# Kernel tuning notes

Hardware: AMD Instinct MI355X
Metric: run time of the kernel (lower is better)

Reference implementation:

```python
import jax, jax.numpy as jnp
import numpy as np

B, P, G, E = 2, 16, 128, 96
C110, C011, C001 = 4, 2, 1
N, CO = 128, 2

def _pw(x, W, b):
    """1x1 conv of any spatial rank == pointwise channel mixing."""
    y = jnp.einsum('oc,bc...->bo...', W, x)
    return y + b.reshape((1, -1) + (1,) * (y.ndim - 2))

def _hidden(s110, s011, s001, Ws, bs):
    # s110:[B,C,P,G,1]  s011:[B,C,1,G,E]  s001:[B,C,1,1,E]
    # sub-stream order: [110 full, 110 pool-P, 110 pool-G, 011 full, 011 pool-G, 011 pool-E, 001]
    t110 = s110[..., 0]         # [B,C,P,G]
    t011 = s011[:, :, 0]        # [B,C,G,E]
    t001 = s001[:, :, 0, 0]     # [B,C,E]
    s = (_pw(t110, Ws[0], bs[0])[..., None]
         + _pw(t110.max(axis=2), Ws[1], bs[1])[:, :, None, :, None]
         + _pw(t110.max(axis=3), Ws[2], bs[2])[:, :, :, None, None]
         + _pw(t011, Ws[3], bs[3])[:, :, None, :, :]
         + _pw(t011.max(axis=2), Ws[4], bs[4])[:, :, None, None, :]
         + _pw(t011.max(axis=3), Ws[5], bs[5])[:, :, None, :, None]
         + _pw(t001, Ws[6], bs[6])[:, :, None, None, :])
    s = jax.nn.leaky_relu(s)    # [B,N,P,G,E]
    return (jnp.max(s, axis=4, keepdims=True),
            jnp.max(s, axis=2, keepdims=True),
            jnp.max(s, axis=(2, 3), keepdims=True))

def _forward(x110, x011, x001, W0_110, b0_110, W0_011, b0_011, W0_001, b0_001, W1, b1, Wact, bact, Wcrit, bcrit):
    Ws0 = [W0_110[0], W0_110[1], W0_110[2], W0_011[0], W0_011[1], W0_011[2], W0_001]
    bs0 = [b0_110[0], b0_110[1], b0_110[2], b0_011[0], b0_011[1], b0_011[2], b0_001]
    s110, s011, s001 = _hidden(x110, x011, x001, Ws0, bs0)
    s110, s011, s001 = _hidden(s110, s011, s001, list(W1), list(b1))
    t110 = s110[..., 0]  # [B,N,P,G]
    # actor head: eliminate G,E via mean pooling (dim_elimination_max_pooling=False)
    a110 = _pw(t110.mean(axis=3), Wact[0], bact[0])              # [B,CO,P]
    a011 = _pw(s011.mean(axis=(3, 4)), Wact[1], bact[1])         # [B,CO,1]
    a001 = _pw(s001[:, :, :, 0].mean(axis=3), Wact[2], bact[2])  # [B,CO,1]
    actions = jax.nn.leaky_relu(a110 + a011 + a001)              # [B,CO,P]
    # critic head: eliminate G via mean pooling
    c110 = _pw(t110.mean(axis=3), Wcrit[0], bcrit[0])            # [B,CO,P]
    c011 = _pw(s011[:, :, 0].mean(axis=2), Wcrit[1], bcrit[1])   # [B,CO,E]
    c001 = _pw(s001[:, :, 0, 0], Wcrit[2], bcrit[2])             # [B,CO,E]
    v = jax.nn.leaky_relu(c110[:, :, :, None] + (c011 + c001)[:, :, None, :])  # [B,CO,P,E]
    v110 = v.max(axis=3).sum(axis=2)  # stream (1,1,0): max over E, sum over P
    v011 = v.max(axis=2).sum(axis=2)  # streams (0,1,1) and (0,0,1) coincide numerically
    values = (2.0 + v110 + 2.0 * v011).reshape(-1)  # python sum(l, 2) starts at 2
    return actions, values

def setup_inputs() -> dict:
    key = jax.random.key(0)
    ks = jax.random.split(key, 12)
    f32 = jnp.float32
    def w(k, shape, fan):
        return jax.random.normal(k, shape, f32) / np.float32(np.sqrt(fan))
    return {
        'x110': jax.random.normal(ks[0], (B, C110, P, G, 1), f32),
        'x011': jax.random.normal(ks[1], (B, C011, 1, G, E), f32),
        'x001': jax.random.normal(ks[2], (B, C001, 1, 1, E), f32),
        'W0_110': w(ks[3], (3, N, C110), C110), 'b0_110': jnp.zeros((3, N), f32),
        'W0_011': w(ks[4], (3, N, C011), C011), 'b0_011': jnp.zeros((3, N), f32),
        'W0_001': w(ks[5], (N, C001), C001),    'b0_001': jnp.zeros((N,), f32),
        'W1':     w(ks[6], (7, N, N), N),       'b1':     jnp.zeros((7, N), f32),
        'Wact':   w(ks[7], (3, CO, N), N),      'bact':   jnp.zeros((3, CO), f32),
        'Wcrit':  w(ks[8], (3, CO, N), N),      'bcrit':  jnp.zeros((3, CO), f32),
    }

def reference(x110, x011, x001, W0_110, b0_110, W0_011, b0_011, W0_001, b0_001, W1, b1, Wact, bact, Wcrit, bcrit):
    return _forward(x110, x011, x001, W0_110, b0_110, W0_011, b0_011, W0_001, b0_001, W1, b1, Wact, bact, Wcrit, bcrit)
```

## Files before the change

### kernel.cpp

```cpp
#include <hip/hip_runtime.h>
#include <math.h>

#define DEVI __device__ __forceinline__

constexpr int B = 2, P = 16, G = 128, E = 96, N = 128, CO = 2;

DEVI float lrelu(float x) { return x > 0.f ? x : 0.01f * x; }

constexpr int OFF_U1     = 0;
constexpr int OFF_V1     = OFF_U1 + 524288;
constexpr int OFF_MAXPU0 = OFF_V1 + 3145728;
constexpr int OFF_MAXEV0 = OFF_MAXPU0 + 32768;
constexpr int OFF_MP110  = OFF_MAXEV0 + 32768;
constexpr int OFF_MG110  = OFF_MP110 + 32768;
constexpr int OFF_S001A  = OFF_MG110 + 4096;
constexpr int OFF_RMP    = OFF_S001A + 24576;
constexpr int OFF_RMG    = OFF_RMP + 1024;
constexpr int OFF_RME    = OFF_RMG + 128;
constexpr int OFF_RMG011 = OFF_RME + 512;
constexpr int OFF_C1P    = OFF_RMG011 + 384;
constexpr int OFF_BF1G   = OFF_C1P + 4096;
constexpr int OFF_EG1E   = OFF_BF1G + 32768;
constexpr int OFF_M110   = OFF_EG1E + 24576;
constexpr int OFF_M011E  = OFF_M110 + 4096;
constexpr int OFF_S001B  = OFF_M011E + 24576;

__global__ void __launch_bounds__(256) k_layer0(
    const float* __restrict__ x110, const float* __restrict__ x011,
    const float* __restrict__ x001,
    const float* __restrict__ W0_110, const float* __restrict__ b0_110,
    const float* __restrict__ W0_011, const float* __restrict__ b0_011,
    const float* __restrict__ W0_001, const float* __restrict__ b0_001,
    float* __restrict__ maxpU0g, float* __restrict__ maxeV0g,
    float* __restrict__ mp110, float* __restrict__ mg110,
    float* __restrict__ s001a,
    float* __restrict__ rmpG, float* __restrict__ rmgG,
    float* __restrict__ rmeG, float* __restrict__ rmg011G) {
  __shared__ float xs[4 * 16 * 128];
  __shared__ float v0[128 * 97];
  __shared__ float u0[16 * 128];
  __shared__ float rmp[4 * 128], rmgS[4 * 16], rme[2 * 128], rmg011L[2 * 96];
  __shared__ float mpu[128], mev[128], part[256];
  const int bn = blockIdx.x, b = bn >> 7, n = bn & 127, tid = threadIdx.x;

  {
    const float4* xsrc = (const float4*)(x110 + (size_t)b * 8192);
    float4* xdst = (float4*)xs;
#pragma unroll
    for (int k = 0; k < 8; k++) xdst[tid + k * 256] = xsrc[tid + k * 256];
  }
  __syncthreads();
  for (int i = tid; i < 512; i += 256) {
    int c = i >> 7, g = i & 127;
    float m = -INFINITY;
    for (int p = 0; p < P; p++) m = fmaxf(m, xs[(c * 16 + p) * 128 + g]);
    rmp[i] = m;
  }
  if (tid < 64) {
    int c = tid >> 4, p = tid & 15;
    float m = -INFINITY;
    for (int g = 0; g < G; g++) m = fmaxf(m, xs[(c * 16 + p) * 128 + g]);
    rmgS[tid] = m;
  }
  {
    int c = tid >> 7, g = tid & 127;
    const float4* r = (const float4*)(x011 + ((size_t)(b * 2 + c) * 128 + g) * 96);
    float m = -INFINITY;
#pragma unroll
    for (int j = 0; j < 24; j++) {
      float4 v = r[j];
      m = fmaxf(m, fmaxf(fmaxf(v.x, v.y), fmaxf(v.z, v.w)));
    }
    rme[tid] = m;
  }
  if (tid < 192) {
    int c = tid / 96, e = tid % 96;
    const float* pp = x011 + ((size_t)(b * 2 + c) * 128) * 96 + e;
    float m = -INFINITY;
    for (int g = 0; g < G; g++) m = fmaxf(m, pp[g * 96]);
    rmg011L[tid] = m;
  }
  __syncthreads();
  float w0[4], w1[4], w2[4];
#pragma unroll
  for (int cc = 0; cc < 4; cc++) {
    w0[cc] = W0_110[n * 4 + cc];
    w1[cc] = W0_110[512 + n * 4 + cc];
    w2[cc] = W0_110[1024 + n * 4 + cc];
  }
  float we0 = W0_011[512 + n * 2], we1 = W0_011[512 + n * 2 + 1];
  float bu = b0_110[n] + b0_110[128 + n] + b0_110[256 + n] + b0_011[256 + n];
  float vw00 = W0_011[n * 2], vw01 = W0_011[n * 2 + 1];
  float vw10 = W0_011[256 + n * 2], vw11 = W0_011[256 + n * 2 + 1];
  float w001 = W0_001[n];
  float bv = b0_011[n] + b0_011[128 + n] + b0_001[n];

#pragma unroll
  for (int k = 0; k < 8; k++) {
    int i = tid + k * 256, p = i >> 7, g = i & 127;
    float acc = bu + we0 * rme[g] + we1 * rme[128 + g];
#pragma unroll
    for (int cc = 0; cc < 4; cc++)
      acc += w0[cc] * xs[(cc * 16 + p) * 128 + g] + w1[cc] * rmp[cc * 128 + g]
           + w2[cc] * rmgS[cc * 16 + p];
    u0[i] = acc;
  }
  {
    const float* xa = x011 + (size_t)(b * 2) * 12288;
    const float* xb = xa + 12288;
    const float* xc = x001 + b * 96;
    for (int k = 0; k < 48; k++) {
      int i = tid + k * 256;
      int g = i / 96, e = i - g * 96;
      float val = bv + vw00 * xa[i] + vw01 * xb[i]
                + vw10 * rmg011L[e] + vw11 * rmg011L[96 + e] + w001 * xc[e];
      v0[g * 97 + e] = val;
    }
  }
  __syncthreads();
  if (tid < 128) {
    float m = -INFINITY;
    for (int p = 0; p < P; p++) m = fmaxf(m, u0[p * 128 + tid]);
    mpu[tid] = m;
    maxpU0g[bn * 128 + tid] = m;
  }
  {
    int g = tid & 127, h = tid >> 7;
    const float* r = &v0[g * 97 + h * 48];
    float m = -INFINITY;
    for (int j = 0; j < 48; j++) m = fmaxf(m, r[j]);
    part[tid] = m;
  }
  __syncthreads();
  if (tid < 128) {
    float m = fmaxf(part[tid], part[128 + tid]);
    mev[tid] = m;
    maxeV0g[bn * 128 + tid] = m;
    mp110[bn * 128 + tid] = lrelu(mpu[tid] + m);
  }
  __syncthreads();
  {
    int p = tid >> 4, ch = tid & 15;
    float m = -INFINITY;
    for (int g = ch * 8; g < ch * 8 + 8; g++)
      m = fmaxf(m, u0[p * 128 + g] + mev[g]);
    part[tid] = m;
  }
  if (tid < 96) {
    float m = -INFINITY;
    for (int g = 0; g < G; g++) m = fmaxf(m, mpu[g] + v0[g * 97 + tid]);
    s001a[bn * 96 + tid] = lrelu(m);
  }
  __syncthreads();
  if (tid < 16) {
    float m = -INFINITY;
    for (int ch = 0; ch < 16; ch++) m = fmaxf(m, part[tid * 16 + ch]);
    mg110[bn * 16 + tid] = lrelu(m);
  }
  if (n == 0) {
    for (int i = tid; i < 512; i += 256) rmpG[b * 512 + i] = rmp[i];
    if (tid < 64) rmgG[b * 64 + tid] = rmgS[tid];
    rmeG[b * 256 + tid] = rme[tid];
    if (tid < 192) rmg011G[b * 192 + tid] = rmg011L[tid];
  }
}

__global__ void k_sg(const float* __restrict__ W1, const float* __restrict__ mp110,
                     const float* __restrict__ mg110, const float* __restrict__ s001a,
                     float* __restrict__ C1p, float* __restrict__ BF1g,
                     float* __restrict__ EG1e) {
  int t = blockIdx.x * 256 + threadIdx.x;
  if (t < 4096) {
    int p = t & 15, n = (t >> 4) & 127, b = t >> 11;
    float acc = 0.f;
    for (int c = 0; c < N; c++)
      acc += W1[(2 * N + n) * N + c] * mg110[(b * N + c) * P + p];
    C1p[t] = acc;
  } else if (t < 36864) {
    int i = t - 4096;
    int g = i & 127, n = (i >> 7) & 127, b = i >> 14;
    float acc = 0.f;
    for (int c = 0; c < N; c++)
      acc += (W1[(1 * N + n) * N + c] + W1[(5 * N + n) * N + c])
             * mp110[(b * N + c) * G + g];
    BF1g[i] = acc;
  } else {
    int i = t - 36864;
    int e = i % 96; int r = i / 96; int n = r & 127, b = r >> 7;
    float acc = 0.f;
    for (int c = 0; c < N; c++)
      acc += (W1[(4 * N + n) * N + c] + W1[(6 * N + n) * N + c])
             * s001a[(b * N + c) * E + e];
    EG1e[i] = acc;
  }
}

__global__ void __launch_bounds__(256) k_layer1(
    const float* __restrict__ x110, const float* __restrict__ x011,
    const float* __restrict__ x001,
    const float* __restrict__ W0_110, const float* __restrict__ b0_110,
    const float* __restrict__ W0_011, const float* __restrict__ b0_011,
    const float* __restrict__ W0_001, const float* __restrict__ b0_001,
    const float* __restrict__ maxpU0g, const float* __restrict__ maxeV0g,
    const float* __restrict__ rmpG, const float* __restrict__ rmgG,
    const float* __restrict__ rmeG, const float* __restrict__ rmg011G,
    const float* __restrict__ W1, const float* __restrict__ b1,
    const float* __restrict__ C1p, const float* __restrict__ BF1g,
    const float* __restrict__ EG1e,
    float* __restrict__ U1, float* __restrict__ V1) {
  __shared__ float s110c[128 * 16];
  __shared__ float s011c[128 * 96];
  __shared__ float W0L110[1536], W0L011[768], W0L001[128];
  __shared__ float busum[128], bvsum[128], mpu[128], mev[128];
  __shared__ float x011row[192], rmg011s[192], x001s[96];
  __shared__ float x110col[64], rmg110p[64], rmp4[4], rme2[2];
  const int blk = blockIdx.x;
  const int b = blk >> 8, g = (blk >> 1) & 127, nh = blk & 1;
  const int n0 = nh * 64;
  const int tid = threadIdx.x;

  for (int i = tid; i < 1536; i += 256) W0L110[i] = W0_110[i];
  for (int i = tid; i < 768; i += 256) W0L011[i] = W0_011[i];
  if (tid < 128) {
    W0L001[tid] = W0_001[tid];
    busum[tid] = b0_110[tid] + b0_110[128 + tid] + b0_110[256 + tid] + b0_011[256 + tid];
    bvsum[tid] = b0_011[tid] + b0_011[128 + tid] + b0_001[tid];
    mpu[tid] = maxpU0g[(b * 128 + tid) * 128 + g];
    mev[tid] = maxeV0g[(b * 128 + tid) * 128 + g];
  }
  if (tid < 192) {
    int c = tid / 96, e = tid % 96;
    x011row[tid] = x011[((size_t)(b * 2 + c) * 128 + g) * 96 + e];
    rmg011s[tid] = rmg011G[b * 192 + tid];
  }
  if (tid < 96) x001s[tid] = x001[b * 96 + tid];
  if (tid < 64) {
    int c = tid >> 4, p = tid & 15;
    x110col[tid] = x110[((size_t)(b * 4 + c) * 16 + p) * 128 + g];
    rmg110p[tid] = rmgG[b * 64 + tid];
  }
  if (tid < 4) rmp4[tid] = rmpG[(b * 4 + tid) * 128 + g];
  if (tid < 2) rme2[tid] = rmeG[(b * 2 + tid) * 128 + g];
  __syncthreads();

#pragma unroll
  for (int k = 0; k < 8; k++) {
    int i = tid + k * 256, c = i >> 4, p = i & 15;
    float acc = busum[c] + W0L011[512 + c * 2] * rme2[0]
              + W0L011[512 + c * 2 + 1] * rme2[1];
#pragma unroll
    for (int cc = 0; cc < 4; cc++)
      acc += W0L110[c * 4 + cc] * x110col[cc * 16 + p]
           + W0L110[512 + c * 4 + cc] * rmp4[cc]
           + W0L110[1024 + c * 4 + cc] * rmg110p[cc * 16 + p];
    s110c[i] = lrelu(acc + mev[c]);
  }
  for (int k = 0; k < 48; k++) {
    int i = tid + k * 256;
    int c = i / 96, e = i - c * 96;
    float v = bvsum[c] + W0L011[c * 2] * x011row[e] + W0L011[c * 2 + 1] * x011row[96 + e]
            + W0L011[256 + c * 2] * rmg011s[e] + W0L011[256 + c * 2 + 1] * rmg011s[96 + e]
            + W0L001[c] * x001s[e];
    s011c[i] = lrelu(v + mpu[c]);
  }
  __syncthreads();

  {
    int nn = tid >> 2, pq = tid & 3;
    int n = n0 + nn;
    float bb = b1[n] + b1[128 + n] + b1[256 + n] + b1[640 + n]
             + BF1g[(b * 128 + n) * 128 + g];
    float4 cp = *(const float4*)&C1p[(b * 128 + n) * 16 + pq * 4];
    float4 a = make_float4(bb + cp.x, bb + cp.y, bb + cp.z, bb + cp.w);
    const float* wr = W1 + (size_t)n * 128;
    for (int c = 0; c < 128; c++) {
      float wv = wr[c];
      float4 s = *(const float4*)&s110c[c * 16 + pq * 4];
      a.x += wv * s.x; a.y += wv * s.y; a.z += wv * s.z; a.w += wv * s.w;
    }
    float* dst = U1 + ((size_t)(b * 128 + n) * 16 + pq * 4) * 128 + g;
    dst[0] = a.x; dst[128] = a.y; dst[256] = a.z; dst[384] = a.w;
  }
  {
    int n2 = tid >> 3, e0 = (tid & 7) * 12;
    int na = n0 + n2 * 2, nb = na + 1;
    float4 aA[3], aB[3];
    {
      float bbA = b1[384 + na] + b1[512 + na] + b1[768 + na];
      float bbB = b1[384 + nb] + b1[512 + nb] + b1[768 + nb];
      const float* egA = EG1e + (b * 128 + na) * 96 + e0;
      const float* egB = EG1e + (b * 128 + nb) * 96 + e0;
#pragma unroll
      for (int k = 0; k < 3; k++) {
        aA[k] = make_float4(bbA + egA[k * 4], bbA + egA[k * 4 + 1],
                            bbA + egA[k * 4 + 2], bbA + egA[k * 4 + 3]);
        aB[k] = make_float4(bbB + egB[k * 4], bbB + egB[k * 4 + 1],
                            bbB + egB[k * 4 + 2], bbB + egB[k * 4 + 3]);
      }
    }
    const float* wA = W1 + (size_t)(384 + na) * 128;
    const float* wB = W1 + (size_t)(384 + nb) * 128;
#pragma unroll 4
    for (int c = 0; c < 128; c++) {
      float4 s0 = *(const float4*)&s011c[c * 96 + e0];
      float4 s1 = *(const float4*)&s011c[c * 96 + e0 + 4];
      float4 s2 = *(const float4*)&s011c[c * 96 + e0 + 8];
      float wa = wA[c], wb = wB[c];
      aA[0].x += wa * s0.x; aA[0].y += wa * s0.y; aA[0].z += wa * s0.z; aA[0].w += wa * s0.w;
      aA[1].x += wa * s1.x; aA[1].y += wa * s1.y; aA[1].z += wa * s1.z; aA[1].w += wa * s1.w;
      aA[2].x += wa * s2.x; aA[2].y += wa * s2.y; aA[2].z += wa * s2.z; aA[2].w += wa * s2.w;
      aB[0].x += wb * s0.x; aB[0].y += wb * s0.y; aB[0].z += wb * s0.z; aB[0].w += wb * s0.w;
      aB[1].x += wb * s1.x; aB[1].y += wb * s1.y; aB[1].z += wb * s1.z; aB[1].w += wb * s1.w;
      aB[2].x += wb * s2.x; aB[2].y += wb * s2.y; aB[2].z += wb * s2.z; aB[2].w += wb * s2.w;
    }
    float* dA = V1 + ((size_t)(b * 128 + na) * 128 + g) * 96 + e0;
    float* dB = V1 + ((size_t)(b * 128 + nb) * 128 + g) * 96 + e0;
#pragma unroll
    for (int k = 0; k < 3; k++) {
      *(float4*)(dA + k * 4) = aA[k];
      *(float4*)(dB + k * 4) = aB[k];
    }
  }
}

__global__ void __launch_bounds__(256) k_post1(
    const float* __restrict__ U1, const float* __restrict__ V1,
    float* __restrict__ m110, float* __restrict__ m011e,
    float* __restrict__ s001b) {
  __shared__ float uU[P * G];
  __shared__ float part[256];
  __shared__ float smaxeV[G], smaxpU[G];
  const int bn = blockIdx.x;
  const int tid = threadIdx.x;
  const float4* usrc = (const float4*)(U1 + (size_t)bn * P * G);
  float4* udst = (float4*)uU;
  udst[tid] = usrc[tid];
  udst[tid + 256] = usrc[tid + 256];
  {
    int g = tid & 127, h = tid >> 7;
    const float* vrow = V1 + ((size_t)bn * G + g) * E + h * 48;
    float m = -INFINITY;
#pragma unroll
    for (int j = 0; j < 12; j++) {
      float4 v = *(const float4*)(vrow + j * 4);
      m = fmaxf(m, fmaxf(fmaxf(v.x, v.y), fmaxf(v.z, v.w)));
    }
    part[tid] = m;
  }
  __syncthreads();
  if (tid < G) {
    smaxeV[tid] = fmaxf(part[tid], part[tid + 128]);
    float mp = -INFINITY;
    for (int p = 0; p < P; p++) mp = fmaxf(mp, uU[p * G + tid]);
    smaxpU[tid] = mp;
  }
  __syncthreads();
  if (tid < P) {
    float s = 0.f;
    for (int g = 0; g < G; g++) s += lrelu(uU[tid * G + g] + smaxeV[g]);
    m110[bn * P + tid] = s * (1.f / G);
  }
  if (tid < E) {
    float s = 0.f, mm = -INFINITY;
    const float* vcol = V1 + (size_t)bn * G * E + tid;
    for (int g = 0; g < G; g++) {
      float pre = smaxpU[g] + vcol[g * E];
      s += lrelu(pre);
      mm = fmaxf(mm, pre);
    }
    m011e[bn * E + tid] = s * (1.f / G);
    s001b[bn * E + tid] = lrelu(mm);
  }
}

__global__ void __launch_bounds__(128) k_final(const float* __restrict__ m110,
                                               const float* __restrict__ m011e,
                                               const float* __restrict__ s001,
                                               const float* __restrict__ Wact,
                                               const float* __restrict__ bact,
                                               const float* __restrict__ Wcrit,
                                               const float* __restrict__ bcrit,
                                               float* __restrict__ out) {
  __shared__ float sm011[N], sm001[N], scp[P], sce[E], srow[P], scol[E];
  const int bo = blockIdx.x;
  const int o = bo & 1, b = bo >> 1;
  const int t = threadIdx.x;
  {
    float s1 = 0.f, s2 = 0.f;
    const float* p1 = m011e + (b * N + t) * E;
    const float* p2 = s001 + (b * N + t) * E;
    for (int e = 0; e < E; e++) { s1 += p1[e]; s2 += p2[e]; }
    sm011[t] = s1 * (1.f / E);
    sm001[t] = s2 * (1.f / E);
  }
  __syncthreads();
  if (t < P) {
    const float* wa0 = Wact + o * N;
    const float* wa1 = Wact + (1 * CO + o) * N;
    const float* wa2 = Wact + (2 * CO + o) * N;
    const float* wc0 = Wcrit + o * N;
    float a = 0.f, c = 0.f, aa = 0.f;
    for (int n = 0; n < N; n++) {
      float m = m110[(b * N + n) * P + t];
      a += wa0[n] * m;
      c += wc0[n] * m;
      aa += wa1[n] * sm011[n] + wa2[n] * sm001[n];
    }
    float act = a + aa + bact[o] + bact[CO + o] + bact[2 * CO + o];
    out[(b * CO + o) * P + t] = lrelu(act);
    scp[t] = c + bcrit[o];
  } else if (t < P + E) {
    int e = t - P;
    const float* wc1 = Wcrit + (1 * CO + o) * N;
    const float* wc2 = Wcrit + (2 * CO + o) * N;
    float c = 0.f;
    for (int n = 0; n < N; n++)
      c += wc1[n] * m011e[(b * N + n) * E + e] + wc2[n] * s001[(b * N + n) * E + e];
    sce[e] = c + bcrit[CO + o] + bcrit[2 * CO + o];
  }
  __syncthreads();
  if (t < P) {
    float m = -INFINITY;
    for (int e = 0; e < E; e++) m = fmaxf(m, lrelu(scp[t] + sce[e]));
    srow[t] = m;
  } else if (t < P + E) {
    int e = t - P;
    float m = -INFINITY;
    for (int p = 0; p < P; p++) m = fmaxf(m, lrelu(scp[p] + sce[e]));
    scol[e] = m;
  }
  __syncthreads();
  if (t == 0) {
    float v110 = 0.f, v011 = 0.f;
    for (int p = 0; p < P; p++) v110 += srow[p];
    for (int e = 0; e < E; e++) v011 += scol[e];
    out[B * CO * P + b * CO + o] = 2.f + v110 + 2.f * v011;
  }
}

extern "C" void kernel_launch(void* const* d_in, const int* in_sizes, int n_in,
                              void* d_out, int out_size, void* d_ws, size_t ws_size,
                              hipStream_t stream) {
  const float* x110   = (const float*)d_in[0];
  const float* x011   = (const float*)d_in[1];
  const float* x001   = (const float*)d_in[2];
  const float* W0_110 = (const float*)d_in[3];
  const float* b0_110 = (const float*)d_in[4];
  const float* W0_011 = (const float*)d_in[5];
  const float* b0_011 = (const float*)d_in[6];
  const float* W0_001 = (const float*)d_in[7];
  const float* b0_001 = (const float*)d_in[8];
  const float* W1     = (const float*)d_in[9];
  const float* b1     = (const float*)d_in[10];
  const float* Wact   = (const float*)d_in[11];
  const float* bact   = (const float*)d_in[12];
  const float* Wcrit  = (const float*)d_in[13];
  const float* bcrit  = (const float*)d_in[14];
  float* out = (float*)d_out;
  float* w = (float*)d_ws;

  float* U1     = w + OFF_U1;
  float* V1     = w + OFF_V1;
  float* maxpU0 = w + OFF_MAXPU0;
  float* maxeV0 = w + OFF_MAXEV0;
  float* mp110  = w + OFF_MP110;
  float* mg110  = w + OFF_MG110;
  float* s001a  = w + OFF_S001A;
  float* rmpG   = w + OFF_RMP;
  float* rmgG   = w + OFF_RMG;
  float* rmeG   = w + OFF_RME;
  float* rmg011 = w + OFF_RMG011;
  float* C1p    = w + OFF_C1P;
  float* BF1g   = w + OFF_BF1G;
  float* EG1e   = w + OFF_EG1E;
  float* m110   = w + OFF_M110;
  float* m011e  = w + OFF_M011E;
  float* s001b  = w + OFF_S001B;

  k_layer0<<<256, 256, 0, stream>>>(x110, x011, x001, W0_110, b0_110, W0_011,
                                    b0_011, W0_001, b0_001,
                                    maxpU0, maxeV0, mp110, mg110, s001a,
                                    rmpG, rmgG, rmeG, rmg011);
  k_sg<<<240, 256, 0, stream>>>(W1, mp110, mg110, s001a, C1p, BF1g, EG1e);
  k_layer1<<<512, 256, 0, stream>>>(x110, x011, x001, W0_110, b0_110, W0_011,
                                    b0_011, W0_001, b0_001,
                                    maxpU0, maxeV0, rmpG, rmgG, rmeG, rmg011,
                                    W1, b1, C1p, BF1g, EG1e, U1, V1);
  k_post1<<<256, 256, 0, stream>>>(U1, V1, m110, m011e, s001b);
  k_final<<<4, 128, 0, stream>>>(m110, m011e, s001b, Wact, bact, Wcrit, bcrit, out);
}
```

Measured before the change: 104.7 us.

## Fold side-stream GEMMs into layer-1 kernel with pre-transposed weights

Removes the separate k_sg kernel. Its small matmuls (C1p, BF1g, EG1e) are now computed inside a reworked layer-1 kernel that runs 256 blocks, one per (b,g), instead of 512. Layer 0 additionally writes a transposed and pre-summed copy of W1 so the layer-1 inner loops read weights coalesced across n. U1 and V1 change layout to g-major, so the post kernel now gathers through strided loads into padded shared memory. This saves one launch and the intermediate round trips, at the cost of more per-block work, fewer blocks and a less coalesced gather in k_post1.

```diff
diff --git a/kernel.cpp b/kernel.cpp
--- a/kernel.cpp
+++ b/kernel.cpp
@@ -18,12 +18,10 @@
 constexpr int OFF_RMG    = OFF_RMP + 1024;
 constexpr int OFF_RME    = OFF_RMG + 128;
 constexpr int OFF_RMG011 = OFF_RME + 512;
-constexpr int OFF_C1P    = OFF_RMG011 + 384;
-constexpr int OFF_BF1G   = OFF_C1P + 4096;
-constexpr int OFF_EG1E   = OFF_BF1G + 32768;
-constexpr int OFF_M110   = OFF_EG1E + 24576;
+constexpr int OFF_M110   = OFF_RMG011 + 384;
 constexpr int OFF_M011E  = OFF_M110 + 4096;
 constexpr int OFF_S001B  = OFF_M011E + 24576;
+constexpr int OFF_WT     = OFF_S001B + 24576;
 
 __global__ void __launch_bounds__(256) k_layer0(
     const float* __restrict__ x110, const float* __restrict__ x011,
@@ -31,15 +29,17 @@
     const float* __restrict__ W0_110, const float* __restrict__ b0_110,
     const float* __restrict__ W0_011, const float* __restrict__ b0_011,
     const float* __restrict__ W0_001, const float* __restrict__ b0_001,
+    const float* __restrict__ W1,
     float* __restrict__ maxpU0g, float* __restrict__ maxeV0g,
     float* __restrict__ mp110, float* __restrict__ mg110,
     float* __restrict__ s001a,
     float* __restrict__ rmpG, float* __restrict__ rmgG,
-    float* __restrict__ rmeG, float* __restrict__ rmg011G) {
+    float* __restrict__ rmeG, float* __restrict__ rmg011G,
+    float* __restrict__ wT) {
   __shared__ float xs[4 * 16 * 128];
   __shared__ float v0[128 * 97];
   __shared__ float u0[16 * 128];
-  __shared__ float rmp[4 * 128], rmgS[4 * 16], rme[2 * 128], rmg011L[2 * 96];
+  __shared__ float rmp[512], rmgS[64], rme[256], rmg011L[192];
   __shared__ float mpu[128], mev[128], part[256];
   const int bn = blockIdx.x, b = bn >> 7, n = bn & 127, tid = threadIdx.x;
 
@@ -163,39 +163,27 @@
     rmeG[b * 256 + tid] = rme[tid];
     if (tid < 192) rmg011G[b * 192 + tid] = rmg011L[tid];
   }
+  {
+    const int gt = bn * 256 + tid;
+#pragma unroll
+    for (int it = 0; it < 2; it++) {
+      int idx = gt + it * 65536;
+      if (idx < 81920) {
+        int m = idx >> 14, r = idx & 16383;
+        int c = r >> 7, nn = r & 127;
+        float v;
+        if (m == 0)      v = W1[nn * 128 + c];
+        else if (m == 1) v = W1[16384 + nn * 128 + c] + W1[5 * 16384 + nn * 128 + c];
+        else if (m == 2) v = W1[2 * 16384 + nn * 128 + c];
+        else if (m == 3) v = W1[3 * 16384 + nn * 128 + c];
+        else             v = W1[4 * 16384 + nn * 128 + c] + W1[6 * 16384 + nn * 128 + c];
+        wT[idx] = v;
+      }
+    }
+  }
 }
 
-__global__ void k_sg(const float* __restrict__ W1, const float* __restrict__ mp110,
-                     const float* __restrict__ mg110, const float* __restrict__ s001a,
-                     float* __restrict__ C1p, float* __restrict__ BF1g,
-                     float* __restrict__ EG1e) {
-  int t = blockIdx.x * 256 + threadIdx.x;
-  if (t < 4096) {
-    int p = t & 15, n = (t >> 4) & 127, b = t >> 11;
-    float acc = 0.f;
-    for (int c = 0; c < N; c++)
-      acc += W1[(2 * N + n) * N + c] * mg110[(b * N + c) * P + p];
-    C1p[t] = acc;
-  } else if (t < 36864) {
-    int i = t - 4096;
-    int g = i & 127, n = (i >> 7) & 127, b = i >> 14;
-    float acc = 0.f;
-    for (int c = 0; c < N; c++)
-      acc += (W1[(1 * N + n) * N + c] + W1[(5 * N + n) * N + c])
-             * mp110[(b * N + c) * G + g];
-    BF1g[i] = acc;
-  } else {
-    int i = t - 36864;
-    int e = i % 96; int r = i / 96; int n = r & 127, b = r >> 7;
-    float acc = 0.f;
-    for (int c = 0; c < N; c++)
-      acc += (W1[(4 * N + n) * N + c] + W1[(6 * N + n) * N + c])
-             * s001a[(b * N + c) * E + e];
-    EG1e[i] = acc;
-  }
-}
-
-__global__ void __launch_bounds__(256) k_layer1(
+__global__ void __launch_bounds__(256) k_layer1b(
     const float* __restrict__ x110, const float* __restrict__ x011,
     const float* __restrict__ x001,
     const float* __restrict__ W0_110, const float* __restrict__ b0_110,
@@ -204,26 +192,33 @@
     const float* __restrict__ maxpU0g, const float* __restrict__ maxeV0g,
     const float* __restrict__ rmpG, const float* __restrict__ rmgG,
     const float* __restrict__ rmeG, const float* __restrict__ rmg011G,
-    const float* __restrict__ W1, const float* __restrict__ b1,
-    const float* __restrict__ C1p, const float* __restrict__ BF1g,
-    const float* __restrict__ EG1e,
+    const float* __restrict__ mp110, const float* __restrict__ mg110,
+    const float* __restrict__ s001a,
+    const float* __restrict__ wT, const float* __restrict__ b1,
     float* __restrict__ U1, float* __restrict__ V1) {
   __shared__ float s110c[128 * 16];
   __shared__ float s011c[128 * 96];
+  __shared__ float sA[128 * 96];
   __shared__ float W0L110[1536], W0L011[768], W0L001[128];
   __shared__ float busum[128], bvsum[128], mpu[128], mev[128];
   __shared__ float x011row[192], rmg011s[192], x001s[96];
   __shared__ float x110col[64], rmg110p[64], rmp4[4], rme2[2];
   const int blk = blockIdx.x;
-  const int b = blk >> 8, g = (blk >> 1) & 127, nh = blk & 1;
-  const int n0 = nh * 64;
+  const int b = blk >> 7, g = blk & 127;
   const int tid = threadIdx.x;
 
   for (int i = tid; i < 1536; i += 256) W0L110[i] = W0_110[i];
   for (int i = tid; i < 768; i += 256) W0L011[i] = W0_011[i];
+  {
+    const float4* src = (const float4*)(s001a + (size_t)b * 12288);
+    float4* dst = (float4*)sA;
+#pragma unroll
+    for (int k = 0; k < 12; k++) dst[tid + k * 256] = src[tid + k * 256];
+  }
   if (tid < 128) {
     W0L001[tid] = W0_001[tid];
-    busum[tid] = b0_110[tid] + b0_110[128 + tid] + b0_110[256 + tid] + b0_011[256 + tid];
+    busum[tid] = b0_110[tid] + b0_110[128 + tid] + b0_110[256 + tid]
+               + b0_011[256 + tid];
     bvsum[tid] = b0_011[tid] + b0_011[128 + tid] + b0_001[tid];
     mpu[tid] = maxpU0g[(b * 128 + tid) * 128 + g];
     mev[tid] = maxeV0g[(b * 128 + tid) * 128 + g];
@@ -258,67 +253,83 @@
   for (int k = 0; k < 48; k++) {
     int i = tid + k * 256;
     int c = i / 96, e = i - c * 96;
-    float v = bvsum[c] + W0L011[c * 2] * x011row[e] + W0L011[c * 2 + 1] * x011row[96 + e]
-            + W0L011[256 + c * 2] * rmg011s[e] + W0L011[256 + c * 2 + 1] * rmg011s[96 + e]
+    float v = bvsum[c]
+            + W0L011[c * 2] * x011row[e] + W0L011[c * 2 + 1] * x011row[96 + e]
+            + W0L011[256 + c * 2] * rmg011s[e]
+            + W0L011[256 + c * 2 + 1] * rmg011s[96 + e]
             + W0L001[c] * x001s[e];
     s011c[i] = lrelu(v + mpu[c]);
   }
   __syncthreads();
 
-  {
-    int nn = tid >> 2, pq = tid & 3;
-    int n = n0 + nn;
-    float bb = b1[n] + b1[128 + n] + b1[256 + n] + b1[640 + n]
-             + BF1g[(b * 128 + n) * 128 + g];
-    float4 cp = *(const float4*)&C1p[(b * 128 + n) * 16 + pq * 4];
-    float4 a = make_float4(bb + cp.x, bb + cp.y, bb + cp.z, bb + cp.w);
-    const float* wr = W1 + (size_t)n * 128;
+  const float* w0T  = wT;
+  const float* w15T = wT + 16384;
+  const float* w2T  = wT + 2 * 16384;
+  const float* w3T  = wT + 3 * 16384;
+  const float* w46T = wT + 4 * 16384;
+
+  {
+    int n = tid & 127, ph = tid >> 7;
+    float bfv = 0.f;
+    float a[8];
+#pragma unroll
+    for (int j = 0; j < 8; j++) a[j] = 0.f;
+    float cp[8];
+#pragma unroll
+    for (int j = 0; j < 8; j++) cp[j] = 0.f;
     for (int c = 0; c < 128; c++) {
-      float wv = wr[c];
-      float4 s = *(const float4*)&s110c[c * 16 + pq * 4];
-      a.x += wv * s.x; a.y += wv * s.y; a.z += wv * s.z; a.w += wv * s.w;
-    }
-    float* dst = U1 + ((size_t)(b * 128 + n) * 16 + pq * 4) * 128 + g;
-    dst[0] = a.x; dst[128] = a.y; dst[256] = a.z; dst[384] = a.w;
-  }
-  {
-    int n2 = tid >> 3, e0 = (tid & 7) * 12;
-    int na = n0 + n2 * 2, nb = na + 1;
-    float4 aA[3], aB[3];
-    {
-      float bbA = b1[384 + na] + b1[512 + na] + b1[768 + na];
-      float bbB = b1[384 + nb] + b1[512 + nb] + b1[768 + nb];
-      const float* egA = EG1e + (b * 128 + na) * 96 + e0;
-      const float* egB = EG1e + (b * 128 + nb) * 96 + e0;
-#pragma unroll
-      for (int k = 0; k < 3; k++) {
-        aA[k] = make_float4(bbA + egA[k * 4], bbA + egA[k * 4 + 1],
-                            bbA + egA[k * 4 + 2], bbA + egA[k * 4 + 3]);
-        aB[k] = make_float4(bbB + egB[k * 4], bbB + egB[k * 4 + 1],
-                            bbB + egB[k * 4 + 2], bbB + egB[k * 4 + 3]);
+      float w0v = w0T[c * 128 + n];
+      float w15v = w15T[c * 128 + n];
+      float w2v = w2T[c * 128 + n];
+      bfv += w15v * mp110[(b * 128 + c) * 128 + g];
+      const float* mgr = &mg110[(b * 128 + c) * 16 + ph * 8];
+      const float* sr = &s110c[c * 16 + ph * 8];
+#pragma unroll
+      for (int j = 0; j < 8; j++) {
+        cp[j] += w2v * mgr[j];
+        a[j] += w0v * sr[j];
       }
     }
-    const float* wA = W1 + (size_t)(384 + na) * 128;
-    const float* wB = W1 + (size_t)(384 + nb) * 128;
-#pragma unroll 4
+    float bb = b1[n] + b1[128 + n] + b1[256 + n] + b1[640 + n] + bfv;
+    float* dst = U1 + ((size_t)((b * 128 + g) * 16 + ph * 8)) * 128 + n;
+#pragma unroll
+    for (int j = 0; j < 8; j++) dst[j * 128] = a[j] + bb + cp[j];
+  }
+  {
+    int n0 = (tid >> 3) * 4, e0 = (tid & 7) * 12;
+    float4 acc[4][3];
+#pragma unroll
+    for (int ni = 0; ni < 4; ni++) {
+      float bbv = b1[384 + n0 + ni] + b1[512 + n0 + ni] + b1[768 + n0 + ni];
+#pragma unroll
+      for (int k = 0; k < 3; k++) acc[ni][k] = make_float4(bbv, bbv, bbv, bbv);
+    }
     for (int c = 0; c < 128; c++) {
+      float4 w3v = *(const float4*)&w3T[c * 128 + n0];
+      float4 w46v = *(const float4*)&w46T[c * 128 + n0];
       float4 s0 = *(const float4*)&s011c[c * 96 + e0];
       float4 s1 = *(const float4*)&s011c[c * 96 + e0 + 4];
       float4 s2 = *(const float4*)&s011c[c * 96 + e0 + 8];
-      float wa = wA[c], wb = wB[c];
-      aA[0].x += wa * s0.x; aA[0].y += wa * s0.y; aA[0].z += wa * s0.z; aA[0].w += wa * s0.w;
-      aA[1].x += wa * s1.x; aA[1].y += wa * s1.y; aA[1].z += wa * s1.z; aA[1].w += wa * s1.w;
-      aA[2].x += wa * s2.x; aA[2].y += wa * s2.y; aA[2].z += wa * s2.z; aA[2].w += wa * s2.w;
-      aB[0].x += wb * s0.x; aB[0].y += wb * s0.y; aB[0].z += wb * s0.z; aB[0].w += wb * s0.w;
-      aB[1].x += wb * s1.x; aB[1].y += wb * s1.y; aB[1].z += wb * s1.z; aB[1].w += wb * s1.w;
-      aB[2].x += wb * s2.x; aB[2].y += wb * s2.y; aB[2].z += wb * s2.z; aB[2].w += wb * s2.w;
-    }
-    float* dA = V1 + ((size_t)(b * 128 + na) * 128 + g) * 96 + e0;
-    float* dB = V1 + ((size_t)(b * 128 + nb) * 128 + g) * 96 + e0;
-#pragma unroll
-    for (int k = 0; k < 3; k++) {
-      *(float4*)(dA + k * 4) = aA[k];
-      *(float4*)(dB + k * 4) = aB[k];
+      float4 t0 = *(const float4*)&sA[c * 96 + e0];
+      float4 t1 = *(const float4*)&sA[c * 96 + e0 + 4];
+      float4 t2 = *(const float4*)&sA[c * 96 + e0 + 8];
+#pragma unroll
+      for (int ni = 0; ni < 4; ni++) {
+        float wa = ni == 0 ? w3v.x : ni == 1 ? w3v.y : ni == 2 ? w3v.z : w3v.w;
+        float wb = ni == 0 ? w46v.x : ni == 1 ? w46v.y : ni == 2 ? w46v.z : w46v.w;
+        acc[ni][0].x += wa * s0.x + wb * t0.x; acc[ni][0].y += wa * s0.y + wb * t0.y;
+        acc[ni][0].z += wa * s0.z + wb * t0.z; acc[ni][0].w += wa * s0.w + wb * t0.w;
+        acc[ni][1].x += wa * s1.x + wb * t1.x; acc[ni][1].y += wa * s1.y + wb * t1.y;
+        acc[ni][1].z += wa * s1.z + wb * t1.z; acc[ni][1].w += wa * s1.w + wb * t1.w;
+        acc[ni][2].x += wa * s2.x + wb * t2.x; acc[ni][2].y += wa * s2.y + wb * t2.y;
+        acc[ni][2].z += wa * s2.z + wb * t2.z; acc[ni][2].w += wa * s2.w + wb * t2.w;
+      }
+    }
+#pragma unroll
+    for (int ni = 0; ni < 4; ni++) {
+      float* dst = V1 + ((size_t)((b * 128 + g) * 128 + n0 + ni)) * 96 + e0;
+#pragma unroll
+      for (int k = 0; k < 3; k++) *(float4*)(dst + k * 4) = acc[ni][k];
     }
   }
 }
@@ -327,49 +338,56 @@
     const float* __restrict__ U1, const float* __restrict__ V1,
     float* __restrict__ m110, float* __restrict__ m011e,
     float* __restrict__ s001b) {
-  __shared__ float uU[P * G];
+  __shared__ float vrow[128 * 97];
+  __shared__ float uU[16 * 128];
   __shared__ float part[256];
-  __shared__ float smaxeV[G], smaxpU[G];
-  const int bn = blockIdx.x;
+  __shared__ float smaxeV[128], smaxpU[128];
+  const int bn = blockIdx.x, b = bn >> 7, n = bn & 127;
   const int tid = threadIdx.x;
-  const float4* usrc = (const float4*)(U1 + (size_t)bn * P * G);
-  float4* udst = (float4*)uU;
-  udst[tid] = usrc[tid];
-  udst[tid + 256] = usrc[tid + 256];
+  for (int i = tid; i < 2048; i += 256) {
+    int p = i >> 7, g = i & 127;
+    uU[i] = U1[((size_t)((b * 128 + g) * 16 + p)) * 128 + n];
+  }
+#pragma unroll
+  for (int k = 0; k < 12; k++) {
+    int i4 = tid + k * 256;
+    int g = i4 / 24, e4 = i4 - g * 24;
+    float4 v = *(const float4*)(V1 + ((size_t)((b * 128 + g) * 128 + n)) * 96 + e4 * 4);
+    float* d = &vrow[g * 97 + e4 * 4];
+    d[0] = v.x; d[1] = v.y; d[2] = v.z; d[3] = v.w;
+  }
+  __syncthreads();
   {
     int g = tid & 127, h = tid >> 7;
-    const float* vrow = V1 + ((size_t)bn * G + g) * E + h * 48;
-    float m = -INFINITY;
-#pragma unroll
-    for (int j = 0; j < 12; j++) {
-      float4 v = *(const float4*)(vrow + j * 4);
-      m = fmaxf(m, fmaxf(fmaxf(v.x, v.y), fmaxf(v.z, v.w)));
-    }
+    const float* r = &vrow[g * 97 + h * 48];
+    float m = -INFINITY;
+    for (int j = 0; j < 48; j++) m = fmaxf(m, r[j]);
     part[tid] = m;
   }
   __syncthreads();
-  if (tid < G) {
+  if (tid < 128) {
     smaxeV[tid] = fmaxf(part[tid], part[tid + 128]);
     float mp = -INFINITY;
-    for (int p = 0; p < P; p++) mp = fmaxf(mp, uU[p * G + tid]);
+    for (int p = 0; p < P; p++) mp = fmaxf(mp, uU[p * 128 + tid]);
     smaxpU[tid] = mp;
   }
   __syncthreads();
-  if (tid < P) {
+  if (tid >= 128 && tid < 144) {
+    int p = tid - 128;
     float s = 0.f;
-    for (int g = 0; g < G; g++) s += lrelu(uU[tid * G + g] + smaxeV[g]);
-    m110[bn * P + tid] = s * (1.f / G);
-  }
-  if (tid < E) {
+    for (int g = 0; g < G; g++)
+      s += lrelu(uU[p * 128 + g] + smaxeV[g]);
+    m110[bn * 16 + p] = s * (1.f / G);
+  }
+  if (tid < 96) {
     float s = 0.f, mm = -INFINITY;
-    const float* vcol = V1 + (size_t)bn * G * E + tid;
     for (int g = 0; g < G; g++) {
-      float pre = smaxpU[g] + vcol[g * E];
+      float pre = smaxpU[g] + vrow[g * 97 + tid];
       s += lrelu(pre);
       mm = fmaxf(mm, pre);
     }
-    m011e[bn * E + tid] = s * (1.f / G);
-    s001b[bn * E + tid] = lrelu(mm);
+    m011e[bn * 96 + tid] = s * (1.f / G);
+    s001b[bn * 96 + tid] = lrelu(mm);
   }
 }
 
@@ -470,22 +488,19 @@
   float* rmgG   = w + OFF_RMG;
   float* rmeG   = w + OFF_RME;
   float* rmg011 = w + OFF_RMG011;
-  float* C1p    = w + OFF_C1P;
-  float* BF1g   = w + OFF_BF1G;
-  float* EG1e   = w + OFF_EG1E;
   float* m110   = w + OFF_M110;
   float* m011e  = w + OFF_M011E;
   float* s001b  = w + OFF_S001B;
+  float* wT     = w + OFF_WT;
 
   k_layer0<<<256, 256, 0, stream>>>(x110, x011, x001, W0_110, b0_110, W0_011,
-                                    b0_011, W0_001, b0_001,
+                                    b0_011, W0_001, b0_001, W1,
                                     maxpU0, maxeV0, mp110, mg110, s001a,
-                                    rmpG, rmgG, rmeG, rmg011);
-  k_sg<<<240, 256, 0, stream>>>(W1, mp110, mg110, s001a, C1p, BF1g, EG1e);
-  k_layer1<<<512, 256, 0, stream>>>(x110, x011, x001, W0_110, b0_110, W0_011,
-                                    b0_011, W0_001, b0_001,
-                                    maxpU0, maxeV0, rmpG, rmgG, rmeG, rmg011,
-                                    W1, b1, C1p, BF1g, EG1e, U1, V1);
+                                    rmpG, rmgG, rmeG, rmg011, wT);
+  k_layer1b<<<256, 256, 0, stream>>>(x110, x011, x001, W0_110, b0_110, W0_011,
+                                     b0_011, W0_001, b0_001,
+                                     maxpU0, maxeV0, rmpG, rmgG, rmeG, rmg011,
+                                     mp110, mg110, s001a, wT, b1, U1, V1);
   k_post1<<<256, 256, 0, stream>>>(U1, V1, m110, m011e, s001b);
   k_final<<<4, 128, 0, stream>>>(m110, m011e, s001b, Wact, bact, Wcrit, bcrit, out);
 }
```

After: 162.8 us. +55.5%, slower.
